# Kernel optimization log

Measured on AMD Instinct MI355X. Metric: run time of the kernel, lower is better.

The kernel has to match this reference:

```python
import jax, jax.numpy as jnp
import numpy as np

N = 50000      # nodes
E = 800000     # edges
D = 128        # hidden_dim == out_dim
VOCAB = 50000  # in_size


def setup_inputs() -> dict:
    key = jax.random.key(0)
    ks = jax.random.split(key, 8)
    batch = jax.random.randint(ks[0], (N,), 0, VOCAB)
    src = jax.random.randint(ks[1], (E,), 0, N)
    dst = jax.random.randint(ks[2], (E,), 0, N)
    emb = jax.random.normal(ks[3], (VOCAB, D), dtype=jnp.float32) * 0.02
    s = 1.0 / np.sqrt(D)
    W1 = jax.random.normal(ks[4], (D, D), dtype=jnp.float32) * s
    W2 = jax.random.normal(ks[5], (D, D), dtype=jnp.float32) * s
    W3 = jax.random.normal(ks[6], (D, D), dtype=jnp.float32) * s
    b1 = jnp.zeros((D,), jnp.float32)
    b2 = jnp.zeros((D,), jnp.float32)
    b3 = jnp.zeros((D,), jnp.float32)
    return {"batch": batch, "src": src, "dst": dst, "emb": emb,
            "W1": W1, "b1": b1, "W2": W2, "b2": b2, "W3": W3, "b3": b3}


def reference(batch, src, dst, emb, W1, b1, W2, b2, W3, b3):
    # embedding lookup over node ids
    x = emb[batch]  # [N, D]
    ones = jnp.ones((E,), x.dtype)
    # DGL GraphConv norm='both': symmetric normalization, degrees clamped >= 1
    deg_out = jnp.clip(jax.ops.segment_sum(ones, src, num_segments=N), 1.0)
    deg_in = jnp.clip(jax.ops.segment_sum(ones, dst, num_segments=N), 1.0)
    norm_src = deg_out ** -0.5  # [N]
    norm_dst = deg_in ** -0.5   # [N]

    def gcn_layer(h, W, b):
        m = (h * norm_src[:, None])[src]                       # gather src messages [E, D]
        agg = jax.ops.segment_sum(m, dst, num_segments=N)      # SpMM aggregate [N, D]
        agg = agg * norm_dst[:, None]
        # dropout p=0.0 is identity; activation is ReLU
        return jax.nn.relu(agg @ W + b)

    x = gcn_layer(x, W1, b1)
    x = gcn_layer(x, W2, b2)
    x = gcn_layer(x, W3, b3)
    return x
```

## Files before the change

### kernel.cpp

```cpp
#include <hip/hip_runtime.h>
#include <math.h>

typedef float f4 __attribute__((ext_vector_type(4)));
typedef float f32x4 __attribute__((ext_vector_type(4)));
typedef short s8 __attribute__((ext_vector_type(8)));
typedef short s4 __attribute__((ext_vector_type(4)));

static constexpr int N = 50000;
static constexpr int E = 800000;
static constexpr int D = 128;
static constexpr int SCAN_NB = (N + 255) / 256;
static constexpr int MBLK = 64;
static constexpr int GRID_M = (N + MBLK - 1) / MBLK;
static constexpr int N_PAD = GRID_M * MBLK;
static constexpr int WT_PITCH = 136;

__device__ inline unsigned short f32_bf16_rne(float x) {
    unsigned u = __float_as_uint(x);
    return (unsigned short)((u + 0x7FFF + ((u >> 16) & 1)) >> 16);
}
__device__ inline float bf16_f32(unsigned short h) {
    return __uint_as_float((unsigned)h << 16);
}

__global__ void deg_kernel(const int* __restrict__ src, const int* __restrict__ dst,
                           int* __restrict__ deg_out, int* __restrict__ deg_in) {
    int e = blockIdx.x * 256 + threadIdx.x;
    if (e < E) {
        atomicAdd(&deg_out[src[e]], 1);
        atomicAdd(&deg_in[dst[e]], 1);
    }
}

__global__ void norm_kernel(const int* __restrict__ deg_out, const int* __restrict__ deg_in,
                            float* __restrict__ norm_src, float* __restrict__ norm_dst) {
    int i = blockIdx.x * 256 + threadIdx.x;
    if (i < N) {
        norm_src[i] = rsqrtf(fmaxf((float)deg_out[i], 1.0f));
        norm_dst[i] = rsqrtf(fmaxf((float)deg_in[i], 1.0f));
    }
}

__global__ __launch_bounds__(256) void scan_bsum_kernel(const int* __restrict__ deg,
                                                        int* __restrict__ bsums) {
    int i = blockIdx.x * 256 + threadIdx.x;
    int v = (i < N) ? deg[i] : 0;
#pragma unroll
    for (int off = 1; off < 64; off <<= 1) v += __shfl_xor(v, off, 64);
    __shared__ int ws[4];
    if ((threadIdx.x & 63) == 0) ws[threadIdx.x >> 6] = v;
    __syncthreads();
    if (threadIdx.x == 0) bsums[blockIdx.x] = ws[0] + ws[1] + ws[2] + ws[3];
}

__global__ __launch_bounds__(256) void scan_bsums_kernel(int* __restrict__ bsums) {
    __shared__ int s[256];
    int t = threadIdx.x;
    s[t] = (t < SCAN_NB) ? bsums[t] : 0;
    __syncthreads();
    for (int off = 1; off < 256; off <<= 1) {
        int v = (t >= off) ? s[t - off] : 0;
        __syncthreads();
        s[t] += v;
        __syncthreads();
    }
    if (t < SCAN_NB) bsums[t] = (t == 0) ? 0 : s[t - 1];
}

__global__ __launch_bounds__(256) void scan_final_kernel(const int* __restrict__ deg,
                                                         const int* __restrict__ bsums,
                                                         int* __restrict__ row_ptr) {
    __shared__ int s[256];
    int b = blockIdx.x, t = threadIdx.x;
    int i = b * 256 + t;
    s[t] = (i < N) ? deg[i] : 0;
    __syncthreads();
    for (int off = 1; off < 256; off <<= 1) {
        int v = (t >= off) ? s[t - off] : 0;
        __syncthreads();
        s[t] += v;
        __syncthreads();
    }
    if (i < N) row_ptr[i + 1] = s[t] + bsums[b];
    if (i == 0) row_ptr[0] = 0;
}

__global__ void fill_kernel(const int* __restrict__ src, const int* __restrict__ dst,
                            const int* __restrict__ row_ptr, int* __restrict__ cursor,
                            int* __restrict__ csr_src) {
    int e = blockIdx.x * 256 + threadIdx.x;
    if (e < E) {
        int d = dst[e];
        int pos = row_ptr[d] + atomicAdd(&cursor[d], 1);
        csr_src[pos] = src[e];
    }
}

__global__ void gather_kernel(const int* __restrict__ batch, const float* __restrict__ emb,
                              const float* __restrict__ norm_src, float* __restrict__ hs) {
    int gid = blockIdx.x * 256 + threadIdx.x;
    int i = gid >> 5;
    int c = (gid & 31) << 2;
    if (i < N) {
        float s = norm_src[i];
        f4 v = *(const f4*)(emb + (size_t)batch[i] * D + c);
        *(f4*)(hs + (size_t)i * D + c) = v * s;
    }
}

__global__ void agg_kernel(const int* __restrict__ row_ptr, const int* __restrict__ csr_src,
                           const float* __restrict__ hs,
                           short* __restrict__ agg_h, short* __restrict__ agg_l) {
    int gid = blockIdx.x * 256 + threadIdx.x;
    int node = gid >> 6;
    if (node >= N) return;
    int lane = threadIdx.x & 63;
    int grp = lane >> 5;
    int col = (lane & 31) << 2;
    int beg = row_ptr[node], end = row_ptr[node + 1];

    f4 a0 = (f4)0.0f, a1 = (f4)0.0f, a2 = (f4)0.0f, a3 = (f4)0.0f;
    f4 a4 = (f4)0.0f, a5 = (f4)0.0f, a6 = (f4)0.0f, a7 = (f4)0.0f;
    int e = beg + grp;
    for (; e + 14 < end; e += 16) {
        int s0 = csr_src[e];
        int s1 = csr_src[e + 2];
        int s2 = csr_src[e + 4];
        int s3 = csr_src[e + 6];
        int s4 = csr_src[e + 8];
        int s5 = csr_src[e + 10];
        int s6 = csr_src[e + 12];
        int s7 = csr_src[e + 14];
        a0 += *(const f4*)(hs + (size_t)s0 * D + col);
        a1 += *(const f4*)(hs + (size_t)s1 * D + col);
        a2 += *(const f4*)(hs + (size_t)s2 * D + col);
        a3 += *(const f4*)(hs + (size_t)s3 * D + col);
        a4 += *(const f4*)(hs + (size_t)s4 * D + col);
        a5 += *(const f4*)(hs + (size_t)s5 * D + col);
        a6 += *(const f4*)(hs + (size_t)s6 * D + col);
        a7 += *(const f4*)(hs + (size_t)s7 * D + col);
    }
    for (; e < end; e += 2)
        a0 += *(const f4*)(hs + (size_t)csr_src[e] * D + col);
    a0 += a1; a2 += a3; a4 += a5; a6 += a7;
    a0 += a2; a4 += a6;
    a0 += a4;

    f4 o;
#pragma unroll
    for (int j = 0; j < 4; ++j)
        o[j] = a0[j] + __shfl_xor(a0[j], 32, 64);
    if (grp == 0) {
        s4 oh, ol;
#pragma unroll
        for (int j = 0; j < 4; ++j) {
            unsigned short h = f32_bf16_rne(o[j]);
            oh[j] = (short)h;
            ol[j] = (short)f32_bf16_rne(o[j] - bf16_f32(h));
        }
        *(s4*)(agg_h + (size_t)node * D + col) = oh;
        *(s4*)(agg_l + (size_t)node * D + col) = ol;
    }
}

__global__ void wprep_kernel(const float* __restrict__ W1, const float* __restrict__ W2,
                             const float* __restrict__ W3, short* __restrict__ wt) {
    int idx = blockIdx.x * 256 + threadIdx.x;
    if (idx >= 3 * D * D) return;
    int l = idx >> 14;
    int e = idx & (D * D - 1);
    int n = e >> 7, k = e & 127;
    const float* W = (l == 0) ? W1 : ((l == 1) ? W2 : W3);
    float w = W[(size_t)k * D + n];
    unsigned short h = f32_bf16_rne(w);
    unsigned short lo = f32_bf16_rne(w - bf16_f32(h));
    wt[(size_t)l * 2 * D * D + (size_t)n * D + k] = (short)h;
    wt[(size_t)l * 2 * D * D + D * D + (size_t)n * D + k] = (short)lo;
}

__global__ __launch_bounds__(256, 2) void gemm_mfma_kernel(
    const short* __restrict__ Ah, const short* __restrict__ Al,
    const short* __restrict__ wth,
    const float* __restrict__ bias, const float* __restrict__ norm_dst,
    const float* __restrict__ post, float* __restrict__ out) {
    __shared__ short wt_h[D * WT_PITCH];
    __shared__ short wt_l[D * WT_PITCH];

    int tid = threadIdx.x;
    const short* gh = wth;
    const short* gl = wth + (size_t)D * D;

#pragma unroll
    for (int it = 0; it < 8; ++it) {
        int c = tid + it * 256;
        int n = c >> 4, kc = c & 15;
        *(s8*)(&wt_h[n * WT_PITCH + kc * 8]) = *(const s8*)(gh + (size_t)n * D + kc * 8);
        *(s8*)(&wt_l[n * WT_PITCH + kc * 8]) = *(const s8*)(gl + (size_t)n * D + kc * 8);
    }
    __syncthreads();

    int wv = tid >> 6;
    int lane = tid & 63;
    int lg = lane >> 4;
    int lr = lane & 15;

    int arow = blockIdx.x * 64 + wv * 16 + lr;
    const short* ahp = Ah + (size_t)arow * D;
    const short* alp = Al + (size_t)arow * D;

    f32x4 acc[8];
#pragma unroll
    for (int nt = 0; nt < 8; ++nt) acc[nt] = (f32x4)0.0f;

#pragma unroll
    for (int kt = 0; kt < 4; ++kt) {
        int ko = kt * 32 + lg * 8;
        s8 ah = *(const s8*)(ahp + ko);
        s8 al = *(const s8*)(alp + ko);
#pragma unroll
        for (int nt = 0; nt < 8; ++nt) {
            int bidx = (nt * 16 + lr) * WT_PITCH + ko;
            s8 bh = *(const s8*)(&wt_h[bidx]);
            s8 bl = *(const s8*)(&wt_l[bidx]);
            acc[nt] = __builtin_amdgcn_mfma_f32_16x16x32_bf16(ah, bh, acc[nt], 0, 0, 0);
            acc[nt] = __builtin_amdgcn_mfma_f32_16x16x32_bf16(al, bh, acc[nt], 0, 0, 0);
            acc[nt] = __builtin_amdgcn_mfma_f32_16x16x32_bf16(ah, bl, acc[nt], 0, 0, 0);
        }
    }

    int r0 = blockIdx.x * 64 + wv * 16 + lg * 4;
    float nd[4], ps[4];
#pragma unroll
    for (int i = 0; i < 4; ++i) {
        int gr = r0 + i;
        nd[i] = (gr < N) ? norm_dst[gr] : 0.0f;
        ps[i] = (gr < N) ? (post ? post[gr] : 1.0f) : 0.0f;
    }
#pragma unroll
    for (int nt = 0; nt < 8; ++nt) {
        int col = nt * 16 + lr;
        float bv = bias[col];
#pragma unroll
        for (int i = 0; i < 4; ++i) {
            int gr = r0 + i;
            if (gr < N) {
                float v = fmaxf(acc[nt][i] * nd[i] + bv, 0.0f) * ps[i];
                out[(size_t)gr * D + col] = v;
            }
        }
    }
}

extern "C" void kernel_launch(void* const* d_in, const int* in_sizes, int n_in,
                              void* d_out, int out_size, void* d_ws, size_t ws_size,
                              hipStream_t stream) {
    const int*   batch = (const int*)d_in[0];
    const int*   src   = (const int*)d_in[1];
    const int*   dst   = (const int*)d_in[2];
    const float* emb   = (const float*)d_in[3];
    const float* W1    = (const float*)d_in[4];
    const float* b1    = (const float*)d_in[5];
    const float* W2    = (const float*)d_in[6];
    const float* b2    = (const float*)d_in[7];
    const float* W3    = (const float*)d_in[8];
    const float* b3    = (const float*)d_in[9];
    float* out = (float*)d_out;

    float* norm_src = (float*)d_ws;
    float* norm_dst = norm_src + N;
    int*   row_ptr  = (int*)(norm_dst + N);
    int*   csr_src  = row_ptr + (N + 1);
    float* hs       = (float*)(csr_src + E) + 3;
    short* agg_h    = (short*)(hs + (size_t)N_PAD * D);
    short* agg_l    = agg_h + (size_t)N_PAD * D;
    short* wt       = agg_l + (size_t)N_PAD * D;
    int*   deg_out  = (int*)agg_h;
    int*   deg_in   = deg_out + N;
    int*   cursor   = deg_in + N;
    int*   bsums    = cursor + N;

    hipMemsetAsync(deg_out, 0, 3 * (size_t)N * sizeof(int), stream);
    deg_kernel<<<(E + 255) / 256, 256, 0, stream>>>(src, dst, deg_out, deg_in);
    norm_kernel<<<(N + 255) / 256, 256, 0, stream>>>(deg_out, deg_in, norm_src, norm_dst);
    scan_bsum_kernel<<<SCAN_NB, 256, 0, stream>>>(deg_in, bsums);
    scan_bsums_kernel<<<1, 256, 0, stream>>>(bsums);
    scan_final_kernel<<<SCAN_NB, 256, 0, stream>>>(deg_in, bsums, row_ptr);
    fill_kernel<<<(E + 255) / 256, 256, 0, stream>>>(src, dst, row_ptr, cursor, csr_src);
    gather_kernel<<<((size_t)N * 32 + 255) / 256, 256, 0, stream>>>(batch, emb, norm_src, hs);
    wprep_kernel<<<(3 * D * D + 255) / 256, 256, 0, stream>>>(W1, W2, W3, wt);

    const float* bs[3] = {b1, b2, b3};
    for (int l = 0; l < 3; ++l) {
        bool last = (l == 2);
        agg_kernel<<<((size_t)N * 64 + 255) / 256, 256, 0, stream>>>(
            row_ptr, csr_src, hs, agg_h, agg_l);
        gemm_mfma_kernel<<<GRID_M, 256, 0, stream>>>(
            agg_h, agg_l, wt + (size_t)l * 2 * D * D, bs[l], norm_dst,
            last ? nullptr : norm_src,
            last ? out : hs);
    }
}
```

Baseline: 398.2 us.

## Fuse embedding gather into first aggregation and split agg columns across blocks

Removes the separate gather kernel: the fill kernel now stores per-edge batch ids and source norms, so layer-0 aggregation reads the embedding table directly with per-edge scaling. The norm and block-sum kernels are merged into one. The aggregation kernel is restructured so each block handles half of the feature columns for four nodes, with four edge groups per wavefront, and blocks are interleaved so both column halves of a node group are scheduled close together. This avoids writing and re-reading a full N x D scaled feature buffer and is meant to improve gather locality, at the cost of extra per-edge CSR arrays and a scale multiply in layer 0.

```diff
diff --git a/kernel.cpp b/kernel.cpp
--- a/kernel.cpp
+++ b/kernel.cpp
@@ -14,6 +14,8 @@
 static constexpr int GRID_M = (N + MBLK - 1) / MBLK;
 static constexpr int N_PAD = GRID_M * MBLK;
 static constexpr int WT_PITCH = 136;
+static constexpr int AGG_NB = N / 4;
+static constexpr int AGG_GRID = AGG_NB * 2;
 
 __device__ inline unsigned short f32_bf16_rne(float x) {
     unsigned u = __float_as_uint(x);
@@ -32,19 +34,17 @@
     }
 }
 
-__global__ void norm_kernel(const int* __restrict__ deg_out, const int* __restrict__ deg_in,
-                            float* __restrict__ norm_src, float* __restrict__ norm_dst) {
+__global__ __launch_bounds__(256) void scan_bsum_norm_kernel(
+    const int* __restrict__ deg_out, const int* __restrict__ deg_in,
+    float* __restrict__ norm_src, float* __restrict__ norm_dst,
+    int* __restrict__ bsums) {
     int i = blockIdx.x * 256 + threadIdx.x;
+    int v = 0;
     if (i < N) {
         norm_src[i] = rsqrtf(fmaxf((float)deg_out[i], 1.0f));
         norm_dst[i] = rsqrtf(fmaxf((float)deg_in[i], 1.0f));
-    }
-}
-
-__global__ __launch_bounds__(256) void scan_bsum_kernel(const int* __restrict__ deg,
-                                                        int* __restrict__ bsums) {
-    int i = blockIdx.x * 256 + threadIdx.x;
-    int v = (i < N) ? deg[i] : 0;
+        v = deg_in[i];
+    }
 #pragma unroll
     for (int off = 1; off < 64; off <<= 1) v += __shfl_xor(v, off, 64);
     __shared__ int ws[4];
@@ -86,70 +86,68 @@
 }
 
 __global__ void fill_kernel(const int* __restrict__ src, const int* __restrict__ dst,
+                            const int* __restrict__ batch, const float* __restrict__ norm_src,
                             const int* __restrict__ row_ptr, int* __restrict__ cursor,
-                            int* __restrict__ csr_src) {
+                            int* __restrict__ csr_src, int* __restrict__ csr_batch,
+                            float* __restrict__ csr_norm) {
     int e = blockIdx.x * 256 + threadIdx.x;
     if (e < E) {
+        int s = src[e];
         int d = dst[e];
         int pos = row_ptr[d] + atomicAdd(&cursor[d], 1);
-        csr_src[pos] = src[e];
-    }
-}
-
-__global__ void gather_kernel(const int* __restrict__ batch, const float* __restrict__ emb,
-                              const float* __restrict__ norm_src, float* __restrict__ hs) {
-    int gid = blockIdx.x * 256 + threadIdx.x;
-    int i = gid >> 5;
-    int c = (gid & 31) << 2;
-    if (i < N) {
-        float s = norm_src[i];
-        f4 v = *(const f4*)(emb + (size_t)batch[i] * D + c);
-        *(f4*)(hs + (size_t)i * D + c) = v * s;
-    }
-}
-
-__global__ void agg_kernel(const int* __restrict__ row_ptr, const int* __restrict__ csr_src,
-                           const float* __restrict__ hs,
+        csr_src[pos] = s;
+        csr_batch[pos] = batch[s];
+        csr_norm[pos] = norm_src[s];
+    }
+}
+
+__global__ void agg_kernel(const int* __restrict__ row_ptr, const int* __restrict__ idx,
+                           const float* __restrict__ escale, const float* __restrict__ table,
                            short* __restrict__ agg_h, short* __restrict__ agg_l) {
-    int gid = blockIdx.x * 256 + threadIdx.x;
-    int node = gid >> 6;
-    if (node >= N) return;
+    int bid = blockIdx.x;
+    int nodeblk = (bid >> 3) * 4 + (bid & 3);
+    int half = (bid >> 2) & 1;
+    int node = nodeblk * 4 + (threadIdx.x >> 6);
     int lane = threadIdx.x & 63;
-    int grp = lane >> 5;
-    int col = (lane & 31) << 2;
+    int grp = lane >> 4;
+    int col = half * 64 + (lane & 15) * 4;
     int beg = row_ptr[node], end = row_ptr[node + 1];
 
     f4 a0 = (f4)0.0f, a1 = (f4)0.0f, a2 = (f4)0.0f, a3 = (f4)0.0f;
-    f4 a4 = (f4)0.0f, a5 = (f4)0.0f, a6 = (f4)0.0f, a7 = (f4)0.0f;
     int e = beg + grp;
-    for (; e + 14 < end; e += 16) {
-        int s0 = csr_src[e];
-        int s1 = csr_src[e + 2];
-        int s2 = csr_src[e + 4];
-        int s3 = csr_src[e + 6];
-        int s4 = csr_src[e + 8];
-        int s5 = csr_src[e + 10];
-        int s6 = csr_src[e + 12];
-        int s7 = csr_src[e + 14];
-        a0 += *(const f4*)(hs + (size_t)s0 * D + col);
-        a1 += *(const f4*)(hs + (size_t)s1 * D + col);
-        a2 += *(const f4*)(hs + (size_t)s2 * D + col);
-        a3 += *(const f4*)(hs + (size_t)s3 * D + col);
-        a4 += *(const f4*)(hs + (size_t)s4 * D + col);
-        a5 += *(const f4*)(hs + (size_t)s5 * D + col);
-        a6 += *(const f4*)(hs + (size_t)s6 * D + col);
-        a7 += *(const f4*)(hs + (size_t)s7 * D + col);
-    }
-    for (; e < end; e += 2)
-        a0 += *(const f4*)(hs + (size_t)csr_src[e] * D + col);
-    a0 += a1; a2 += a3; a4 += a5; a6 += a7;
-    a0 += a2; a4 += a6;
-    a0 += a4;
+    if (escale) {
+        for (; e + 12 < end; e += 16) {
+            int s0 = idx[e], s1 = idx[e + 4], s2 = idx[e + 8], s3 = idx[e + 12];
+            float w0 = escale[e], w1 = escale[e + 4];
+            float w2 = escale[e + 8], w3 = escale[e + 12];
+            a0 += *(const f4*)(table + (size_t)s0 * D + col) * w0;
+            a1 += *(const f4*)(table + (size_t)s1 * D + col) * w1;
+            a2 += *(const f4*)(table + (size_t)s2 * D + col) * w2;
+            a3 += *(const f4*)(table + (size_t)s3 * D + col) * w3;
+        }
+        for (; e < end; e += 4)
+            a0 += *(const f4*)(table + (size_t)idx[e] * D + col) * escale[e];
+    } else {
+        for (; e + 12 < end; e += 16) {
+            int s0 = idx[e], s1 = idx[e + 4], s2 = idx[e + 8], s3 = idx[e + 12];
+            a0 += *(const f4*)(table + (size_t)s0 * D + col);
+            a1 += *(const f4*)(table + (size_t)s1 * D + col);
+            a2 += *(const f4*)(table + (size_t)s2 * D + col);
+            a3 += *(const f4*)(table + (size_t)s3 * D + col);
+        }
+        for (; e < end; e += 4)
+            a0 += *(const f4*)(table + (size_t)idx[e] * D + col);
+    }
+    a0 += a1; a2 += a3; a0 += a2;
 
     f4 o;
 #pragma unroll
-    for (int j = 0; j < 4; ++j)
-        o[j] = a0[j] + __shfl_xor(a0[j], 32, 64);
+    for (int j = 0; j < 4; ++j) {
+        float v = a0[j];
+        v += __shfl_xor(v, 16, 64);
+        v += __shfl_xor(v, 32, 64);
+        o[j] = v;
+    }
     if (grp == 0) {
         s4 oh, ol;
 #pragma unroll
@@ -266,34 +264,42 @@
     const float* b3    = (const float*)d_in[9];
     float* out = (float*)d_out;
 
-    float* norm_src = (float*)d_ws;
-    float* norm_dst = norm_src + N;
-    int*   row_ptr  = (int*)(norm_dst + N);
-    int*   csr_src  = row_ptr + (N + 1);
-    float* hs       = (float*)(csr_src + E) + 3;
-    short* agg_h    = (short*)(hs + (size_t)N_PAD * D);
-    short* agg_l    = agg_h + (size_t)N_PAD * D;
-    short* wt       = agg_l + (size_t)N_PAD * D;
-    int*   deg_out  = (int*)agg_h;
-    int*   deg_in   = deg_out + N;
-    int*   cursor   = deg_in + N;
-    int*   bsums    = cursor + N;
+    float* norm_src  = (float*)d_ws;
+    float* norm_dst  = norm_src + N;
+    int*   row_ptr   = (int*)(norm_dst + N);
+    int*   csr_src   = row_ptr + (N + 1);
+    float* hs        = (float*)(csr_src + E) + 3;
+    short* agg_h     = (short*)(hs + (size_t)N_PAD * D);
+    short* agg_l     = agg_h + (size_t)N_PAD * D;
+    short* wt        = agg_l + (size_t)N_PAD * D;
+    int*   csr_batch = (int*)hs;
+    float* csr_norm  = hs + E;
+    int*   deg_out   = (int*)agg_h;
+    int*   deg_in    = deg_out + N;
+    int*   cursor    = deg_in + N;
+    int*   bsums     = cursor + N;
 
     hipMemsetAsync(deg_out, 0, 3 * (size_t)N * sizeof(int), stream);
     deg_kernel<<<(E + 255) / 256, 256, 0, stream>>>(src, dst, deg_out, deg_in);
-    norm_kernel<<<(N + 255) / 256, 256, 0, stream>>>(deg_out, deg_in, norm_src, norm_dst);
-    scan_bsum_kernel<<<SCAN_NB, 256, 0, stream>>>(deg_in, bsums);
+    scan_bsum_norm_kernel<<<SCAN_NB, 256, 0, stream>>>(deg_out, deg_in,
+                                                       norm_src, norm_dst, bsums);
     scan_bsums_kernel<<<1, 256, 0, stream>>>(bsums);
     scan_final_kernel<<<SCAN_NB, 256, 0, stream>>>(deg_in, bsums, row_ptr);
-    fill_kernel<<<(E + 255) / 256, 256, 0, stream>>>(src, dst, row_ptr, cursor, csr_src);
-    gather_kernel<<<((size_t)N * 32 + 255) / 256, 256, 0, stream>>>(batch, emb, norm_src, hs);
+    fill_kernel<<<(E + 255) / 256, 256, 0, stream>>>(src, dst, batch, norm_src,
+                                                     row_ptr, cursor,
+                                                     csr_src, csr_batch, csr_norm);
     wprep_kernel<<<(3 * D * D + 255) / 256, 256, 0, stream>>>(W1, W2, W3, wt);
 
     const float* bs[3] = {b1, b2, b3};
     for (int l = 0; l < 3; ++l) {
         bool last = (l == 2);
-        agg_kernel<<<((size_t)N * 64 + 255) / 256, 256, 0, stream>>>(
-            row_ptr, csr_src, hs, agg_h, agg_l);
+        if (l == 0) {
+            agg_kernel<<<AGG_GRID, 256, 0, stream>>>(
+                row_ptr, csr_batch, csr_norm, emb, agg_h, agg_l);
+        } else {
+            agg_kernel<<<AGG_GRID, 256, 0, stream>>>(
+                row_ptr, csr_src, nullptr, hs, agg_h, agg_l);
+        }
         gemm_mfma_kernel<<<GRID_M, 256, 0, stream>>>(
             agg_h, agg_l, wt + (size_t)l * 2 * D * D, bs[l], norm_dst,
             last ? nullptr : norm_src,
```

After: 394.2 us. About the same (-1.0%).

## Pre-sort edges by source so CSR rows have ordered source indices

Applied to the files above, without the earlier changes.

Adds a source-bucketed counting-sort pass before the destination CSR fill so that neighbor lists within each row come out roughly sorted by source, aiming to improve gather locality in the aggregation kernel. Also fuses the normalization computation into the block-sum scan kernel, which now computes both in- and out-degree block sums. This adds an extra scan and an extra atomic fill pass over all edges, with scratch space aliased into the hs buffer.

```diff
diff --git a/kernel.cpp b/kernel.cpp
--- a/kernel.cpp
+++ b/kernel.cpp
@@ -32,25 +32,34 @@
     }
 }
 
-__global__ void norm_kernel(const int* __restrict__ deg_out, const int* __restrict__ deg_in,
-                            float* __restrict__ norm_src, float* __restrict__ norm_dst) {
+__global__ __launch_bounds__(256) void scan_bsum_norm_kernel(
+    const int* __restrict__ deg_out, const int* __restrict__ deg_in,
+    float* __restrict__ norm_src, float* __restrict__ norm_dst,
+    int* __restrict__ bsums_in, int* __restrict__ bsums_out) {
     int i = blockIdx.x * 256 + threadIdx.x;
+    int vi = 0, vo = 0;
     if (i < N) {
-        norm_src[i] = rsqrtf(fmaxf((float)deg_out[i], 1.0f));
-        norm_dst[i] = rsqrtf(fmaxf((float)deg_in[i], 1.0f));
-    }
-}
-
-__global__ __launch_bounds__(256) void scan_bsum_kernel(const int* __restrict__ deg,
-                                                        int* __restrict__ bsums) {
-    int i = blockIdx.x * 256 + threadIdx.x;
-    int v = (i < N) ? deg[i] : 0;
-#pragma unroll
-    for (int off = 1; off < 64; off <<= 1) v += __shfl_xor(v, off, 64);
-    __shared__ int ws[4];
-    if ((threadIdx.x & 63) == 0) ws[threadIdx.x >> 6] = v;
+        int dgo = deg_out[i], dgi = deg_in[i];
+        norm_src[i] = rsqrtf(fmaxf((float)dgo, 1.0f));
+        norm_dst[i] = rsqrtf(fmaxf((float)dgi, 1.0f));
+        vi = dgi;
+        vo = dgo;
+    }
+#pragma unroll
+    for (int off = 1; off < 64; off <<= 1) {
+        vi += __shfl_xor(vi, off, 64);
+        vo += __shfl_xor(vo, off, 64);
+    }
+    __shared__ int wsi[4], wso[4];
+    if ((threadIdx.x & 63) == 0) {
+        wsi[threadIdx.x >> 6] = vi;
+        wso[threadIdx.x >> 6] = vo;
+    }
     __syncthreads();
-    if (threadIdx.x == 0) bsums[blockIdx.x] = ws[0] + ws[1] + ws[2] + ws[3];
+    if (threadIdx.x == 0) {
+        bsums_in[blockIdx.x] = wsi[0] + wsi[1] + wsi[2] + wsi[3];
+        bsums_out[blockIdx.x] = wso[0] + wso[1] + wso[2] + wso[3];
+    }
 }
 
 __global__ __launch_bounds__(256) void scan_bsums_kernel(int* __restrict__ bsums) {
@@ -69,7 +78,7 @@
 
 __global__ __launch_bounds__(256) void scan_final_kernel(const int* __restrict__ deg,
                                                          const int* __restrict__ bsums,
-                                                         int* __restrict__ row_ptr) {
+                                                         int* __restrict__ ptr) {
     __shared__ int s[256];
     int b = blockIdx.x, t = threadIdx.x;
     int i = b * 256 + t;
@@ -81,18 +90,30 @@
         s[t] += v;
         __syncthreads();
     }
-    if (i < N) row_ptr[i + 1] = s[t] + bsums[b];
-    if (i == 0) row_ptr[0] = 0;
-}
-
-__global__ void fill_kernel(const int* __restrict__ src, const int* __restrict__ dst,
-                            const int* __restrict__ row_ptr, int* __restrict__ cursor,
-                            int* __restrict__ csr_src) {
+    if (i < N) ptr[i + 1] = s[t] + bsums[b];
+    if (i == 0) ptr[0] = 0;
+}
+
+__global__ void fill_a_kernel(const int* __restrict__ src, const int* __restrict__ dst,
+                              const int* __restrict__ srow_ptr, int* __restrict__ scursor,
+                              int* __restrict__ ssrc, int* __restrict__ sdst) {
     int e = blockIdx.x * 256 + threadIdx.x;
     if (e < E) {
-        int d = dst[e];
+        int s = src[e];
+        int spos = srow_ptr[s] + atomicAdd(&scursor[s], 1);
+        ssrc[spos] = s;
+        sdst[spos] = dst[e];
+    }
+}
+
+__global__ void fill_b_kernel(const int* __restrict__ ssrc, const int* __restrict__ sdst,
+                              const int* __restrict__ row_ptr, int* __restrict__ cursor,
+                              int* __restrict__ csr_src) {
+    int i = blockIdx.x * 256 + threadIdx.x;
+    if (i < E) {
+        int d = sdst[i];
         int pos = row_ptr[d] + atomicAdd(&cursor[d], 1);
-        csr_src[pos] = src[e];
+        csr_src[pos] = ssrc[i];
     }
 }
 
@@ -266,27 +287,39 @@
     const float* b3    = (const float*)d_in[9];
     float* out = (float*)d_out;
 
-    float* norm_src = (float*)d_ws;
-    float* norm_dst = norm_src + N;
-    int*   row_ptr  = (int*)(norm_dst + N);
-    int*   csr_src  = row_ptr + (N + 1);
-    float* hs       = (float*)(csr_src + E) + 3;
-    short* agg_h    = (short*)(hs + (size_t)N_PAD * D);
-    short* agg_l    = agg_h + (size_t)N_PAD * D;
-    short* wt       = agg_l + (size_t)N_PAD * D;
-    int*   deg_out  = (int*)agg_h;
-    int*   deg_in   = deg_out + N;
-    int*   cursor   = deg_in + N;
-    int*   bsums    = cursor + N;
-
-    hipMemsetAsync(deg_out, 0, 3 * (size_t)N * sizeof(int), stream);
+    float* norm_src  = (float*)d_ws;
+    float* norm_dst  = norm_src + N;
+    int*   row_ptr   = (int*)(norm_dst + N);
+    int*   csr_src   = row_ptr + (N + 1);
+    float* hs        = (float*)(csr_src + E) + 3;
+    short* agg_h     = (short*)(hs + (size_t)N_PAD * D);
+    short* agg_l     = agg_h + (size_t)N_PAD * D;
+    short* wt        = agg_l + (size_t)N_PAD * D;
+    int*   ssrc      = (int*)hs;
+    int*   sdst      = ssrc + E;
+    int*   deg_out   = (int*)agg_h;
+    int*   deg_in    = deg_out + N;
+    int*   cursor    = deg_in + N;
+    int*   scursor   = cursor + N;
+    int*   bsums_in  = scursor + N;
+    int*   bsums_out = bsums_in + SCAN_NB;
+    int*   srow_ptr  = bsums_out + SCAN_NB;
+
+    hipMemsetAsync(deg_out, 0, 4 * (size_t)N * sizeof(int), stream);
     deg_kernel<<<(E + 255) / 256, 256, 0, stream>>>(src, dst, deg_out, deg_in);
-    norm_kernel<<<(N + 255) / 256, 256, 0, stream>>>(deg_out, deg_in, norm_src, norm_dst);
-    scan_bsum_kernel<<<SCAN_NB, 256, 0, stream>>>(deg_in, bsums);
-    scan_bsums_kernel<<<1, 256, 0, stream>>>(bsums);
-    scan_final_kernel<<<SCAN_NB, 256, 0, stream>>>(deg_in, bsums, row_ptr);
-    fill_kernel<<<(E + 255) / 256, 256, 0, stream>>>(src, dst, row_ptr, cursor, csr_src);
-    gather_kernel<<<((size_t)N * 32 + 255) / 256, 256, 0, stream>>>(batch, emb, norm_src, hs);
+    scan_bsum_norm_kernel<<<SCAN_NB, 256, 0, stream>>>(deg_out, deg_in,
+                                                       norm_src, norm_dst,
+                                                       bsums_in, bsums_out);
+    scan_bsums_kernel<<<1, 256, 0, stream>>>(bsums_in);
+    scan_bsums_kernel<<<1, 256, 0, stream>>>(bsums_out);
+    scan_final_kernel<<<SCAN_NB, 256, 0, stream>>>(deg_in, bsums_in, row_ptr);
+    scan_final_kernel<<<SCAN_NB, 256, 0, stream>>>(deg_out, bsums_out, srow_ptr);
+    fill_a_kernel<<<(E + 255) / 256, 256, 0, stream>>>(src, dst, srow_ptr, scursor,
+                                                       ssrc, sdst);
+    fill_b_kernel<<<(E + 255) / 256, 256, 0, stream>>>(ssrc, sdst, row_ptr, cursor,
+                                                       csr_src);
+    gather_kernel<<<((size_t)N * 32 + 255) / 256, 256, 0, stream>>>(batch, emb,
+                                                                    norm_src, hs);
     wprep_kernel<<<(3 * D * D + 255) / 256, 256, 0, stream>>>(W1, W2, W3, wt);
 
     const float* bs[3] = {b1, b2, b3};
```

Measured after the change: 450.8 us. +13.2%, slower.

## Bucket CSR edges by source-node tile and widen GEMM blocks to 128 rows

Applied to the files above, without the earlier changes.

Builds the CSR with each destination's edges grouped into eight buckets by source-node range. This uses per-(tile,dst) counts, offsets and cursors, so during aggregation the gathers walk source rows in a more local order and may hit L2 better. The aggregation loop now iterates over the buckets with a smaller unroll. The GEMM moves to 128-row blocks of 512 threads. The cost is larger count/offset arrays, more atomics targets and more index loads per node, and the boundary handling changes too.

```diff
diff --git a/kernel.cpp b/kernel.cpp
--- a/kernel.cpp
+++ b/kernel.cpp
@@ -9,8 +9,10 @@
 static constexpr int N = 50000;
 static constexpr int E = 800000;
 static constexpr int D = 128;
+static constexpr int T = 8;
+static constexpr int TS = (N + T - 1) / T;
 static constexpr int SCAN_NB = (N + 255) / 256;
-static constexpr int MBLK = 64;
+static constexpr int MBLK = 128;
 static constexpr int GRID_M = (N + MBLK - 1) / MBLK;
 static constexpr int N_PAD = GRID_M * MBLK;
 static constexpr int WT_PITCH = 136;
@@ -23,28 +25,33 @@
     return __uint_as_float((unsigned)h << 16);
 }
 
-__global__ void deg_kernel(const int* __restrict__ src, const int* __restrict__ dst,
-                           int* __restrict__ deg_out, int* __restrict__ deg_in) {
+__global__ void hist_kernel(const int* __restrict__ src, const int* __restrict__ dst,
+                            int* __restrict__ deg_out, int* __restrict__ cnt) {
     int e = blockIdx.x * 256 + threadIdx.x;
     if (e < E) {
-        atomicAdd(&deg_out[src[e]], 1);
-        atomicAdd(&deg_in[dst[e]], 1);
-    }
-}
-
-__global__ void norm_kernel(const int* __restrict__ deg_out, const int* __restrict__ deg_in,
-                            float* __restrict__ norm_src, float* __restrict__ norm_dst) {
+        int s = src[e];
+        int d = dst[e];
+        atomicAdd(&deg_out[s], 1);
+        int t = s / TS;
+        atomicAdd(&cnt[t * N + d], 1);
+    }
+}
+
+__global__ __launch_bounds__(256) void scan_bsum_norm_kernel(
+    const int* __restrict__ deg_out, const int* __restrict__ cnt,
+    float* __restrict__ norm_src, float* __restrict__ norm_dst,
+    int* __restrict__ bsums) {
     int i = blockIdx.x * 256 + threadIdx.x;
+    int tot = 0;
     if (i < N) {
+        int c = 0;
+#pragma unroll
+        for (int t = 0; t < T; ++t) c += cnt[t * N + i];
+        tot = c;
         norm_src[i] = rsqrtf(fmaxf((float)deg_out[i], 1.0f));
-        norm_dst[i] = rsqrtf(fmaxf((float)deg_in[i], 1.0f));
-    }
-}
-
-__global__ __launch_bounds__(256) void scan_bsum_kernel(const int* __restrict__ deg,
-                                                        int* __restrict__ bsums) {
-    int i = blockIdx.x * 256 + threadIdx.x;
-    int v = (i < N) ? deg[i] : 0;
+        norm_dst[i] = rsqrtf(fmaxf((float)tot, 1.0f));
+    }
+    int v = tot;
 #pragma unroll
     for (int off = 1; off < 64; off <<= 1) v += __shfl_xor(v, off, 64);
     __shared__ int ws[4];
@@ -67,32 +74,48 @@
     if (t < SCAN_NB) bsums[t] = (t == 0) ? 0 : s[t - 1];
 }
 
-__global__ __launch_bounds__(256) void scan_final_kernel(const int* __restrict__ deg,
-                                                         const int* __restrict__ bsums,
-                                                         int* __restrict__ row_ptr) {
+__global__ __launch_bounds__(256) void scan_final_boff_kernel(
+    const int* __restrict__ cnt, const int* __restrict__ bsums,
+    int* __restrict__ boff) {
     __shared__ int s[256];
-    int b = blockIdx.x, t = threadIdx.x;
-    int i = b * 256 + t;
-    s[t] = (i < N) ? deg[i] : 0;
+    int b = blockIdx.x, tid = threadIdx.x;
+    int i = b * 256 + tid;
+    int c[T];
+    int tot = 0;
+    if (i < N) {
+#pragma unroll
+        for (int t = 0; t < T; ++t) { c[t] = cnt[t * N + i]; tot += c[t]; }
+    }
+    s[tid] = tot;
     __syncthreads();
     for (int off = 1; off < 256; off <<= 1) {
-        int v = (t >= off) ? s[t - off] : 0;
+        int v = (tid >= off) ? s[tid - off] : 0;
         __syncthreads();
-        s[t] += v;
+        s[tid] += v;
         __syncthreads();
     }
-    if (i < N) row_ptr[i + 1] = s[t] + bsums[b];
-    if (i == 0) row_ptr[0] = 0;
+    if (i < N) {
+        int run = s[tid] - tot + bsums[b];
+#pragma unroll
+        for (int t = 0; t < T; ++t) {
+            boff[t * N + i] = run;
+            run += c[t];
+        }
+        boff[T * N + i] = run;
+    }
 }
 
 __global__ void fill_kernel(const int* __restrict__ src, const int* __restrict__ dst,
-                            const int* __restrict__ row_ptr, int* __restrict__ cursor,
+                            const int* __restrict__ boff, int* __restrict__ cur,
                             int* __restrict__ csr_src) {
     int e = blockIdx.x * 256 + threadIdx.x;
     if (e < E) {
+        int s = src[e];
         int d = dst[e];
-        int pos = row_ptr[d] + atomicAdd(&cursor[d], 1);
-        csr_src[pos] = src[e];
+        int t = s / TS;
+        int idx = t * N + d;
+        int pos = boff[idx] + atomicAdd(&cur[idx], 1);
+        csr_src[pos] = s;
     }
 }
 
@@ -108,49 +131,41 @@
     }
 }
 
-__global__ void agg_kernel(const int* __restrict__ row_ptr, const int* __restrict__ csr_src,
+__global__ void agg_kernel(const int* __restrict__ boff, const int* __restrict__ csr_src,
                            const float* __restrict__ hs,
                            short* __restrict__ agg_h, short* __restrict__ agg_l) {
     int gid = blockIdx.x * 256 + threadIdx.x;
     int node = gid >> 6;
     if (node >= N) return;
     int lane = threadIdx.x & 63;
-    int grp = lane >> 5;
+    int eg = lane >> 5;
     int col = (lane & 31) << 2;
-    int beg = row_ptr[node], end = row_ptr[node + 1];
-
-    f4 a0 = (f4)0.0f, a1 = (f4)0.0f, a2 = (f4)0.0f, a3 = (f4)0.0f;
-    f4 a4 = (f4)0.0f, a5 = (f4)0.0f, a6 = (f4)0.0f, a7 = (f4)0.0f;
-    int e = beg + grp;
-    for (; e + 14 < end; e += 16) {
-        int s0 = csr_src[e];
-        int s1 = csr_src[e + 2];
-        int s2 = csr_src[e + 4];
-        int s3 = csr_src[e + 6];
-        int s4 = csr_src[e + 8];
-        int s5 = csr_src[e + 10];
-        int s6 = csr_src[e + 12];
-        int s7 = csr_src[e + 14];
-        a0 += *(const f4*)(hs + (size_t)s0 * D + col);
-        a1 += *(const f4*)(hs + (size_t)s1 * D + col);
-        a2 += *(const f4*)(hs + (size_t)s2 * D + col);
-        a3 += *(const f4*)(hs + (size_t)s3 * D + col);
-        a4 += *(const f4*)(hs + (size_t)s4 * D + col);
-        a5 += *(const f4*)(hs + (size_t)s5 * D + col);
-        a6 += *(const f4*)(hs + (size_t)s6 * D + col);
-        a7 += *(const f4*)(hs + (size_t)s7 * D + col);
-    }
-    for (; e < end; e += 2)
-        a0 += *(const f4*)(hs + (size_t)csr_src[e] * D + col);
-    a0 += a1; a2 += a3; a4 += a5; a6 += a7;
-    a0 += a2; a4 += a6;
-    a0 += a4;
+
+    int b[T + 1];
+#pragma unroll
+    for (int t = 0; t <= T; ++t) b[t] = boff[t * N + node];
+
+    f4 a0 = (f4)0.0f, a1 = (f4)0.0f;
+#pragma unroll
+    for (int t = 0; t < T; ++t) {
+        int e = b[t] + eg;
+        int en = b[t + 1];
+        for (; e + 2 < en; e += 4) {
+            int s0 = csr_src[e];
+            int s1 = csr_src[e + 2];
+            a0 += *(const f4*)(hs + (size_t)s0 * D + col);
+            a1 += *(const f4*)(hs + (size_t)s1 * D + col);
+        }
+        if (e < en)
+            a0 += *(const f4*)(hs + (size_t)csr_src[e] * D + col);
+    }
+    a0 += a1;
 
     f4 o;
 #pragma unroll
     for (int j = 0; j < 4; ++j)
         o[j] = a0[j] + __shfl_xor(a0[j], 32, 64);
-    if (grp == 0) {
+    if (eg == 0) {
         s4 oh, ol;
 #pragma unroll
         for (int j = 0; j < 4; ++j) {
@@ -178,7 +193,7 @@
     wt[(size_t)l * 2 * D * D + D * D + (size_t)n * D + k] = (short)lo;
 }
 
-__global__ __launch_bounds__(256, 2) void gemm_mfma_kernel(
+__global__ __launch_bounds__(512, 2) void gemm_mfma_kernel(
     const short* __restrict__ Ah, const short* __restrict__ Al,
     const short* __restrict__ wth,
     const float* __restrict__ bias, const float* __restrict__ norm_dst,
@@ -191,8 +206,8 @@
     const short* gl = wth + (size_t)D * D;
 
 #pragma unroll
-    for (int it = 0; it < 8; ++it) {
-        int c = tid + it * 256;
+    for (int it = 0; it < 4; ++it) {
+        int c = tid + it * 512;
         int n = c >> 4, kc = c & 15;
         *(s8*)(&wt_h[n * WT_PITCH + kc * 8]) = *(const s8*)(gh + (size_t)n * D + kc * 8);
         *(s8*)(&wt_l[n * WT_PITCH + kc * 8]) = *(const s8*)(gl + (size_t)n * D + kc * 8);
@@ -204,7 +219,7 @@
     int lg = lane >> 4;
     int lr = lane & 15;
 
-    int arow = blockIdx.x * 64 + wv * 16 + lr;
+    int arow = blockIdx.x * MBLK + wv * 16 + lr;
     const short* ahp = Ah + (size_t)arow * D;
     const short* alp = Al + (size_t)arow * D;
 
@@ -228,7 +243,7 @@
         }
     }
 
-    int r0 = blockIdx.x * 64 + wv * 16 + lg * 4;
+    int r0 = blockIdx.x * MBLK + wv * 16 + lg * 4;
     float nd[4], ps[4];
 #pragma unroll
     for (int i = 0; i < 4; ++i) {
@@ -268,33 +283,34 @@
 
     float* norm_src = (float*)d_ws;
     float* norm_dst = norm_src + N;
-    int*   row_ptr  = (int*)(norm_dst + N);
-    int*   csr_src  = row_ptr + (N + 1);
-    float* hs       = (float*)(csr_src + E) + 3;
+    int*   boff     = (int*)(norm_dst + N);
+    int*   csr_src  = boff + (size_t)(T + 1) * N;
+    float* hs       = (float*)(csr_src + E);
     short* agg_h    = (short*)(hs + (size_t)N_PAD * D);
     short* agg_l    = agg_h + (size_t)N_PAD * D;
     short* wt       = agg_l + (size_t)N_PAD * D;
     int*   deg_out  = (int*)agg_h;
-    int*   deg_in   = deg_out + N;
-    int*   cursor   = deg_in + N;
-    int*   bsums    = cursor + N;
-
-    hipMemsetAsync(deg_out, 0, 3 * (size_t)N * sizeof(int), stream);
-    deg_kernel<<<(E + 255) / 256, 256, 0, stream>>>(src, dst, deg_out, deg_in);
-    norm_kernel<<<(N + 255) / 256, 256, 0, stream>>>(deg_out, deg_in, norm_src, norm_dst);
-    scan_bsum_kernel<<<SCAN_NB, 256, 0, stream>>>(deg_in, bsums);
+    int*   cnt      = deg_out + N;
+    int*   cur      = cnt + (size_t)T * N;
+    int*   bsums    = cur + (size_t)T * N;
+
+    hipMemsetAsync(deg_out, 0, (size_t)(1 + 2 * T) * N * sizeof(int), stream);
+    hist_kernel<<<(E + 255) / 256, 256, 0, stream>>>(src, dst, deg_out, cnt);
+    scan_bsum_norm_kernel<<<SCAN_NB, 256, 0, stream>>>(deg_out, cnt,
+                                                       norm_src, norm_dst, bsums);
     scan_bsums_kernel<<<1, 256, 0, stream>>>(bsums);
-    scan_final_kernel<<<SCAN_NB, 256, 0, stream>>>(deg_in, bsums, row_ptr);
-    fill_kernel<<<(E + 255) / 256, 256, 0, stream>>>(src, dst, row_ptr, cursor, csr_src);
-    gather_kernel<<<((size_t)N * 32 + 255) / 256, 256, 0, stream>>>(batch, emb, norm_src, hs);
+    scan_final_boff_kernel<<<SCAN_NB, 256, 0, stream>>>(cnt, bsums, boff);
+    fill_kernel<<<(E + 255) / 256, 256, 0, stream>>>(src, dst, boff, cur, csr_src);
+    gather_kernel<<<((size_t)N * 32 + 255) / 256, 256, 0, stream>>>(batch, emb,
+                                                                    norm_src, hs);
     wprep_kernel<<<(3 * D * D + 255) / 256, 256, 0, stream>>>(W1, W2, W3, wt);
 
     const float* bs[3] = {b1, b2, b3};
     for (int l = 0; l < 3; ++l) {
         bool last = (l == 2);
         agg_kernel<<<((size_t)N * 64 + 255) / 256, 256, 0, stream>>>(
-            row_ptr, csr_src, hs, agg_h, agg_l);
-        gemm_mfma_kernel<<<GRID_M, 256, 0, stream>>>(
+            boff, csr_src, hs, agg_h, agg_l);
+        gemm_mfma_kernel<<<GRID_M, 512, 0, stream>>>(
             agg_h, agg_l, wt + (size_t)l * 2 * D * D, bs[l], norm_dst,
             last ? nullptr : norm_src,
             last ? out : hs);
```

Result: no change. 393.2 us (-1.3%).
